# Performance work log

Measured on AMD Instinct MI355X. Metric: run time of the kernel, lower is better.

Reference implementation:

```python
import jax, jax.numpy as jnp
import numpy as np

KY, KX = 3, 3  # kernel_size
PAD_Y = (KY - 1) // 2
PAD_X = (KX - 1) // 2
CENTER = (KY * KX) // 2  # flat index of excluded center tap
CY, CX = CENTER // KX, CENTER % KX


def setup_inputs() -> dict:
    key = jax.random.key(0)
    x = jax.random.normal(key, (8, 4, 2048, 2048), dtype=jnp.float32)
    return {"x": x}


def reference(x):
    # Replicate-padded sliding-window max over the (KY, KX) neighborhood,
    # excluding the center tap (same math as the identity-kernel grouped conv
    # followed by max over the channel-expanded neighborhood axis).
    B, CH, H, W = x.shape
    xp = jnp.pad(x, ((0, 0), (0, 0), (PAD_Y, PAD_Y), (PAD_X, PAD_X)), mode='edge')
    max_non_center = jnp.full_like(x, -jnp.inf)
    for dy in range(KY):
        for dx in range(KX):
            if dy == CY and dx == CX:
                continue  # exclude center
            shifted = jax.lax.dynamic_slice(
                xp, (0, 0, dy, dx), (B, CH, H, W))
            max_non_center = jnp.maximum(max_non_center, shifted)
    mask = x > max_non_center
    return x * mask.astype(x.dtype)
```

## Files before the change

kernel.cpp:

```cpp
#include <hip/hip_runtime.h>


#define IMG_H 2048
#define IMG_W 2048

__global__ __launch_bounds__(256) void nms2d_kernel(const float* __restrict__ x,
                                                    float* __restrict__ out,
                                                    int nplanes) {
    const int wq = IMG_W / 4;
    long long tid = (long long)blockIdx.x * blockDim.x + threadIdx.x;
    long long total = (long long)nplanes * IMG_H * wq;
    if (tid >= total) return;

    int col4  = (int)(tid % wq);
    long long rest = tid / wq;
    int row   = (int)(rest % IMG_H);
    int plane = (int)(rest / IMG_H);

    const float* p = x   + (size_t)plane * IMG_H * IMG_W;
    float*       o = out + (size_t)plane * IMG_H * IMG_W;

    int c0 = col4 * 4;
    int rm = row > 0          ? row - 1 : 0;
    int rp = row < IMG_H - 1  ? row + 1 : IMG_H - 1;
    int cl = c0 > 0           ? c0 - 1  : 0;
    int cr = c0 + 4 < IMG_W   ? c0 + 4  : IMG_W - 1;

    const float* rowt = p + (size_t)rm  * IMG_W;
    const float* rowm = p + (size_t)row * IMG_W;
    const float* rowb = p + (size_t)rp  * IMG_W;

    float4 t = *(const float4*)(rowt + c0);
    float4 m = *(const float4*)(rowm + c0);
    float4 b = *(const float4*)(rowb + c0);
    float tl = rowt[cl], tr = rowt[cr];
    float ml = rowm[cl], mr = rowm[cr];
    float bl = rowb[cl], br = rowb[cr];

    float t0 = fmaxf(fmaxf(tl,  t.x), t.y);
    float t1 = fmaxf(fmaxf(t.x, t.y), t.z);
    float t2 = fmaxf(fmaxf(t.y, t.z), t.w);
    float t3 = fmaxf(fmaxf(t.z, t.w), tr);

    float b0 = fmaxf(fmaxf(bl,  b.x), b.y);
    float b1 = fmaxf(fmaxf(b.x, b.y), b.z);
    float b2 = fmaxf(fmaxf(b.y, b.z), b.w);
    float b3 = fmaxf(fmaxf(b.z, b.w), br);

    float m0 = fmaxf(ml,  m.y);
    float m1 = fmaxf(m.x, m.z);
    float m2 = fmaxf(m.y, m.w);
    float m3 = fmaxf(m.z, mr);

    float x0 = fmaxf(fmaxf(t0, b0), m0);
    float x1 = fmaxf(fmaxf(t1, b1), m1);
    float x2 = fmaxf(fmaxf(t2, b2), m2);
    float x3 = fmaxf(fmaxf(t3, b3), m3);

    float4 r;
    r.x = (m.x > x0) ? m.x : 0.0f;
    r.y = (m.y > x1) ? m.y : 0.0f;
    r.z = (m.z > x2) ? m.z : 0.0f;
    r.w = (m.w > x3) ? m.w : 0.0f;

    *(float4*)(o + (size_t)row * IMG_W + c0) = r;
}

extern "C" void kernel_launch(void* const* d_in, const int* in_sizes, int n_in,
                              void* d_out, int out_size, void* d_ws, size_t ws_size,
                              hipStream_t stream) {
    const float* x = (const float*)d_in[0];
    float* out = (float*)d_out;
    int nplanes = in_sizes[0] / (IMG_H * IMG_W);

    long long total = (long long)nplanes * IMG_H * (IMG_W / 4);
    int blocks = (int)((total + 255) / 256);
    nms2d_kernel<<<blocks, 256, 0, stream>>>(x, out, nplanes);
}
```

Baseline: 900.3 us.

## Process 4 rows per thread and share column halos via wavefront shuffles

Each thread now computes 4 output rows from 6 loaded input rows, reusing the horizontal max of each row across neighbouring outputs, so each thread reads 6 rows instead of 3 per output row. The left and right neighbour values are taken from adjacent lanes with __shfl instead of separate scalar loads, and only the wavefront edge lanes fall back to global loads. This cuts redundant memory traffic and index arithmetic in a bandwidth-bound stencil, at the cost of more registers per thread and fewer blocks in flight.

```diff
diff --git a/kernel.cpp b/kernel.cpp
--- a/kernel.cpp
+++ b/kernel.cpp
@@ -3,67 +3,83 @@
 
 #define IMG_H 2048
 #define IMG_W 2048
+#define ROWS 4
 
 __global__ __launch_bounds__(256) void nms2d_kernel(const float* __restrict__ x,
-                                                    float* __restrict__ out,
-                                                    int nplanes) {
-    const int wq = IMG_W / 4;
-    long long tid = (long long)blockIdx.x * blockDim.x + threadIdx.x;
-    long long total = (long long)nplanes * IMG_H * wq;
-    if (tid >= total) return;
+                                                    float* __restrict__ out) {
+    const int wq   = IMG_W / 4;
+    const int segs = wq / 256;
 
-    int col4  = (int)(tid % wq);
-    long long rest = tid / wq;
-    int row   = (int)(rest % IMG_H);
-    int plane = (int)(rest / IMG_H);
+    int seg   = blockIdx.x % segs;
+    int rest  = blockIdx.x / segs;
+    int rowg  = rest % (IMG_H / ROWS);
+    int plane = rest / (IMG_H / ROWS);
+
+    int col4 = seg * 256 + threadIdx.x;
+    int c0   = col4 * 4;
+    int r0   = rowg * ROWS;
+    int lane = threadIdx.x & 63;
 
     const float* p = x   + (size_t)plane * IMG_H * IMG_W;
     float*       o = out + (size_t)plane * IMG_H * IMG_W;
 
-    int c0 = col4 * 4;
-    int rm = row > 0          ? row - 1 : 0;
-    int rp = row < IMG_H - 1  ? row + 1 : IMG_H - 1;
-    int cl = c0 > 0           ? c0 - 1  : 0;
-    int cr = c0 + 4 < IMG_W   ? c0 + 4  : IMG_W - 1;
+    float4 v[ROWS + 2];
+    int    rr[ROWS + 2];
+    #pragma unroll
+    for (int j = 0; j < ROWS + 2; ++j) {
+        int r = r0 - 1 + j;
+        r = r < 0 ? 0 : (r > IMG_H - 1 ? IMG_H - 1 : r);
+        rr[j] = r;
+        v[j] = *(const float4*)(p + (size_t)r * IMG_W + c0);
+    }
 
-    const float* rowt = p + (size_t)rm  * IMG_W;
-    const float* rowm = p + (size_t)row * IMG_W;
-    const float* rowb = p + (size_t)rp  * IMG_W;
+    float lv[ROWS + 2], rv[ROWS + 2];
+    #pragma unroll
+    for (int j = 0; j < ROWS + 2; ++j) {
+        lv[j] = __shfl(v[j].w, lane - 1);
+        rv[j] = __shfl(v[j].x, lane + 1);
+    }
+    if (lane == 0) {
+        #pragma unroll
+        for (int j = 0; j < ROWS + 2; ++j)
+            lv[j] = (c0 > 0) ? p[(size_t)rr[j] * IMG_W + (c0 - 1)] : v[j].x;
+    }
+    if (lane == 63) {
+        #pragma unroll
+        for (int j = 0; j < ROWS + 2; ++j)
+            rv[j] = (c0 + 4 < IMG_W) ? p[(size_t)rr[j] * IMG_W + (c0 + 4)] : v[j].w;
+    }
 
-    float4 t = *(const float4*)(rowt + c0);
-    float4 m = *(const float4*)(rowm + c0);
-    float4 b = *(const float4*)(rowb + c0);
-    float tl = rowt[cl], tr = rowt[cr];
-    float ml = rowm[cl], mr = rowm[cr];
-    float bl = rowb[cl], br = rowb[cr];
+    float h[ROWS + 2][4];
+    #pragma unroll
+    for (int j = 0; j < ROWS + 2; ++j) {
+        h[j][0] = fmaxf(fmaxf(lv[j],   v[j].x), v[j].y);
+        h[j][1] = fmaxf(fmaxf(v[j].x,  v[j].y), v[j].z);
+        h[j][2] = fmaxf(fmaxf(v[j].y,  v[j].z), v[j].w);
+        h[j][3] = fmaxf(fmaxf(v[j].z,  v[j].w), rv[j]);
+    }
 
-    float t0 = fmaxf(fmaxf(tl,  t.x), t.y);
-    float t1 = fmaxf(fmaxf(t.x, t.y), t.z);
-    float t2 = fmaxf(fmaxf(t.y, t.z), t.w);
-    float t3 = fmaxf(fmaxf(t.z, t.w), tr);
+    #pragma unroll
+    for (int i = 0; i < ROWS; ++i) {
+        const int j = i + 1;
+        float m0 = fmaxf(lv[j],   v[j].y);
+        float m1 = fmaxf(v[j].x,  v[j].z);
+        float m2 = fmaxf(v[j].y,  v[j].w);
+        float m3 = fmaxf(v[j].z,  rv[j]);
 
-    float b0 = fmaxf(fmaxf(bl,  b.x), b.y);
-    float b1 = fmaxf(fmaxf(b.x, b.y), b.z);
-    float b2 = fmaxf(fmaxf(b.y, b.z), b.w);
-    float b3 = fmaxf(fmaxf(b.z, b.w), br);
+        float x0 = fmaxf(fmaxf(h[j - 1][0], h[j + 1][0]), m0);
+        float x1 = fmaxf(fmaxf(h[j - 1][1], h[j + 1][1]), m1);
+        float x2 = fmaxf(fmaxf(h[j - 1][2], h[j + 1][2]), m2);
+        float x3 = fmaxf(fmaxf(h[j - 1][3], h[j + 1][3]), m3);
 
-    float m0 = fmaxf(ml,  m.y);
-    float m1 = fmaxf(m.x, m.z);
-    float m2 = fmaxf(m.y, m.w);
-    float m3 = fmaxf(m.z, mr);
+        float4 r;
+        r.x = (v[j].x > x0) ? v[j].x : 0.0f;
+        r.y = (v[j].y > x1) ? v[j].y : 0.0f;
+        r.z = (v[j].z > x2) ? v[j].z : 0.0f;
+        r.w = (v[j].w > x3) ? v[j].w : 0.0f;
 
-    float x0 = fmaxf(fmaxf(t0, b0), m0);
-    float x1 = fmaxf(fmaxf(t1, b1), m1);
-    float x2 = fmaxf(fmaxf(t2, b2), m2);
-    float x3 = fmaxf(fmaxf(t3, b3), m3);
-
-    float4 r;
-    r.x = (m.x > x0) ? m.x : 0.0f;
-    r.y = (m.y > x1) ? m.y : 0.0f;
-    r.z = (m.z > x2) ? m.z : 0.0f;
-    r.w = (m.w > x3) ? m.w : 0.0f;
-
-    *(float4*)(o + (size_t)row * IMG_W + c0) = r;
+        *(float4*)(o + (size_t)(r0 + i) * IMG_W + c0) = r;
+    }
 }
 
 extern "C" void kernel_launch(void* const* d_in, const int* in_sizes, int n_in,
@@ -73,7 +89,7 @@
     float* out = (float*)d_out;
     int nplanes = in_sizes[0] / (IMG_H * IMG_W);
 
-    long long total = (long long)nplanes * IMG_H * (IMG_W / 4);
-    int blocks = (int)((total + 255) / 256);
-    nms2d_kernel<<<blocks, 256, 0, stream>>>(x, out, nplanes);
+    const int segs = (IMG_W / 4) / 256;
+    long long blocks = (long long)nplanes * (IMG_H / ROWS) * segs;
+    nms2d_kernel<<<(int)blocks, 256, 0, stream>>>(x, out);
 }
```

After: 834.8 us. 7.3% less time.
